# Kernel tuning notes

Hardware: AMD Instinct MI355X
Metric: run time of the kernel (lower is better)

The kernel has to match this reference:

```python
import jax, jax.numpy as jnp
import numpy as np
from jax.scipy.stats import norm

N_TOK, D_MODEL, N_EXP, N_SEL = 16384, 4096, 16, 4
NOISE_EPS = 0.01
LOSS_LAMBDA = 0.01


def setup_inputs() -> dict:
    key = jax.random.key(0)
    kx, k1, k2, kn, kz = jax.random.split(key, 5)
    x = jax.random.normal(kx, (N_TOK, D_MODEL), dtype=jnp.float32)
    w1 = jax.random.normal(k1, (N_EXP, D_MODEL), dtype=jnp.float32) * 0.02
    w2 = jax.random.normal(k2, (N_EXP, N_EXP), dtype=jnp.float32) * 0.02
    wn = jax.random.normal(kn, (N_EXP, D_MODEL), dtype=jnp.float32) * 0.02
    noise = jax.random.normal(kz, (N_TOK, N_EXP), dtype=jnp.float32)
    return {"x": x, "w1": w1, "w2": w2, "wn": wn, "noise": noise}


def _cv_squared(v, eps=1e-10):
    # torch .var() is unbiased (ddof=1)
    return jnp.var(v, ddof=1) / (jnp.mean(v) ** 2 + eps)


def reference(x, w1, w2, wn, noise):
    # MLP gate: Linear(D->E, no bias) -> tanh -> Linear(E->E, no bias)
    logits_gate = jnp.einsum("te,fe->tf", jnp.tanh(jnp.einsum("td,ed->te", x, w1)), w2)
    noise_control = jax.nn.softplus(jnp.einsum("td,ed->te", x, wn)) + NOISE_EPS
    logits_noise = noise * noise_control
    logits = logits_gate + logits_noise  # [T, E]

    m = min(N_SEL + 1, N_EXP)  # k+1 values for threshold computation
    top_logits, top_indices = jax.lax.top_k(logits, m)  # [T, m]
    top_k_logits = top_logits[:, :N_SEL]
    top_k_indices = top_indices[:, :N_SEL]
    top_k_scores = jax.nn.softmax(top_k_logits, axis=1)  # [T, k]

    # importance: scatter top-k scores back to dense [T, E]
    rows = jnp.arange(N_TOK)[:, None]
    scores_filtered = jnp.zeros_like(logits).at[rows, top_k_indices].set(top_k_scores)
    importance = scores_filtered.sum(0)  # [E]

    # load: smooth estimator via Normal CDF (faithful to source, which
    # compares logits_noise against the in/out thresholds)
    threshold_if_in = top_logits[:, N_SEL:N_SEL + 1]       # (k+1)-th top value, [T,1]
    threshold_if_out = top_logits[:, N_SEL - 1:N_SEL]      # k-th top value, [T,1]
    is_in = logits_noise > threshold_if_in
    prob_if_in = norm.cdf((logits_gate - threshold_if_in) / noise_control)
    prob_if_out = norm.cdf((logits_gate - threshold_if_out) / noise_control)
    prob = jnp.where(is_in, prob_if_in, prob_if_out)
    load = prob.sum(0)  # [E]

    gate_loss = LOSS_LAMBDA * (_cv_squared(importance) + _cv_squared(load))
    return top_k_indices, top_k_scores, gate_loss
```

## Files before the change

kernel.cpp:

```cpp
#include <hip/hip_runtime.h>
#include <math.h>

#define N_TOK   16384
#define D_MODEL 4096
#define N_EXP   16
#define N_SEL   4
#define WELEM   (N_EXP * D_MODEL)

typedef __bf16 bf16x8 __attribute__((ext_vector_type(8)));
typedef float  f32x4  __attribute__((ext_vector_type(4)));

#define MFMA(a, b, c) __builtin_amdgcn_mfma_f32_16x16x32_bf16((a), (b), (c), 0, 0, 0)

__global__ __launch_bounds__(256) void wprep_kernel(const float* __restrict__ w1,
                                                    const float* __restrict__ wn,
                                                    __bf16* __restrict__ wbuf,
                                                    float* __restrict__ g_acc)
{
    const int i = blockIdx.x * 256 + threadIdx.x;
    if (blockIdx.x == 0 && threadIdx.x < 2 * N_EXP) g_acc[threadIdx.x] = 0.f;
    {
        const float v = w1[i];
        const __bf16 h = (__bf16)v;  const float r1 = v - (float)h;
        const __bf16 m = (__bf16)r1; const float r2 = r1 - (float)m;
        wbuf[i] = h; wbuf[WELEM + i] = m; wbuf[2 * WELEM + i] = (__bf16)r2;
    }
    {
        const float v = wn[i];
        const __bf16 h = (__bf16)v;  const float r1 = v - (float)h;
        const __bf16 m = (__bf16)r1; const float r2 = r1 - (float)m;
        wbuf[3 * WELEM + i] = h; wbuf[4 * WELEM + i] = m; wbuf[5 * WELEM + i] = (__bf16)r2;
    }
}

__global__ __launch_bounds__(512, 8) void gate_kernel(
    const float* __restrict__ x, const __bf16* __restrict__ wbuf,
    const float* __restrict__ w2, const float* __restrict__ noise,
    float* __restrict__ out, float* __restrict__ g_imp, float* __restrict__ g_load)
{
    __shared__ float red[8][16][32];
    __shared__ float dsum[16][32];
    __shared__ float s_imp[N_EXP], s_ld[N_EXP];

    const int tid  = threadIdx.x;
    const int lane = tid & 63;
    const int wv   = tid >> 6;
    const int ml   = lane & 15;
    const int q    = lane >> 4;
    const int t0   = blockIdx.x * 16;

    const __bf16* w1h = wbuf;
    const __bf16* w1m = wbuf + WELEM;
    const __bf16* w1l = wbuf + 2 * WELEM;
    const __bf16* wnh = wbuf + 3 * WELEM;
    const __bf16* wnm = wbuf + 4 * WELEM;
    const __bf16* wnl = wbuf + 5 * WELEM;

    const size_t xoff = (size_t)(t0 + ml) * D_MODEL + wv * 512 + q * 8;
    const int    woff = ml * D_MODEL + wv * 512 + q * 8;

    f32x4 c1 = {0.f, 0.f, 0.f, 0.f};
    f32x4 c2 = {0.f, 0.f, 0.f, 0.f};

    #pragma unroll 2
    for (int it = 0; it < 16; ++it) {
        const int ko = it * 32;
        const float4 xa = *(const float4*)(x + xoff + ko);
        const float4 xb = *(const float4*)(x + xoff + ko + 4);
        const bf16x8 a1h = *(const bf16x8*)(w1h + woff + ko);
        const bf16x8 a1m = *(const bf16x8*)(w1m + woff + ko);
        const bf16x8 a1l = *(const bf16x8*)(w1l + woff + ko);
        const bf16x8 a2h = *(const bf16x8*)(wnh + woff + ko);
        const bf16x8 a2m = *(const bf16x8*)(wnm + woff + ko);
        const bf16x8 a2l = *(const bf16x8*)(wnl + woff + ko);

        const float xv[8] = {xa.x, xa.y, xa.z, xa.w, xb.x, xb.y, xb.z, xb.w};
        bf16x8 xh, xm8, xl;
        #pragma unroll
        for (int j = 0; j < 8; ++j) {
            const float v  = xv[j];
            const __bf16 h = (__bf16)v;   const float r1 = v - (float)h;
            const __bf16 md = (__bf16)r1; const float r2 = r1 - (float)md;
            xh[j] = h; xm8[j] = md; xl[j] = (__bf16)r2;
        }

        c1 = MFMA(a1h, xh, c1);  c1 = MFMA(a1h, xm8, c1); c1 = MFMA(a1m, xh, c1);
        c1 = MFMA(a1h, xl, c1);  c1 = MFMA(a1l, xh, c1);  c1 = MFMA(a1m, xm8, c1);
        c2 = MFMA(a2h, xh, c2);  c2 = MFMA(a2h, xm8, c2); c2 = MFMA(a2m, xh, c2);
        c2 = MFMA(a2h, xl, c2);  c2 = MFMA(a2l, xh, c2);  c2 = MFMA(a2m, xm8, c2);
    }

    #pragma unroll
    for (int r = 0; r < 4; ++r) {
        red[wv][ml][q * 4 + r]      = c1[r];
        red[wv][ml][16 + q * 4 + r] = c2[r];
    }
    __syncthreads();

    {
        const int tk = tid >> 5, o = tid & 31;
        float s = 0.f;
        #pragma unroll
        for (int w = 0; w < 8; ++w) s += red[w][tk][o];
        dsum[tk][o] = s;
    }
    if (tid < N_EXP) { s_imp[tid] = 0.f; s_ld[tid] = 0.f; }
    __syncthreads();

    if (tid < 16) {
        const int t = t0 + tid;
        float dot[32];
        #pragma unroll
        for (int e = 0; e < 32; ++e) dot[e] = dsum[tid][e];

        float th[N_EXP], nc[N_EXP];
        #pragma unroll
        for (int e = 0; e < N_EXP; ++e) th[e] = tanhf(dot[e]);
        #pragma unroll
        for (int e = 0; e < N_EXP; ++e) {
            const float v = dot[N_EXP + e];
            nc[e] = fmaxf(v, 0.f) + log1pf(expf(-fabsf(v))) + 0.01f;
        }

        float lg[N_EXP];
        #pragma unroll
        for (int f = 0; f < N_EXP; ++f) {
            float s = 0.f;
            #pragma unroll
            for (int e = 0; e < N_EXP; ++e) s = fmaf(th[e], w2[f * 16 + e], s);
            lg[f] = s;
        }

        float ln[N_EXP], v[N_EXP];
        {
            const float4* nz = (const float4*)(noise + (size_t)t * 16);
            const float4 n0 = nz[0], n1 = nz[1], n2 = nz[2], n3 = nz[3];
            const float nzv[16] = {n0.x, n0.y, n0.z, n0.w, n1.x, n1.y, n1.z, n1.w,
                                   n2.x, n2.y, n2.z, n2.w, n3.x, n3.y, n3.z, n3.w};
            #pragma unroll
            for (int e = 0; e < N_EXP; ++e) {
                ln[e] = nzv[e] * nc[e];
                v[e]  = lg[e] + ln[e];
            }
        }

        float tv[5]; int ti[5];
        #pragma unroll
        for (int j = 0; j < 5; ++j) {
            float best = -INFINITY; int bi = 0;
            #pragma unroll
            for (int e = 0; e < N_EXP; ++e) {
                bool taken = false;
                #pragma unroll
                for (int jj = 0; jj < 5; ++jj)
                    if (jj < j) taken = taken || (ti[jj] == e);
                if (!taken && v[e] > best) { best = v[e]; bi = e; }
            }
            tv[j] = best; ti[j] = bi;
        }

        const float mx = tv[0];
        float ex[4], ssum = 0.f;
        #pragma unroll
        for (int j = 0; j < 4; ++j) { ex[j] = expf(tv[j] - mx); ssum += ex[j]; }
        const float inv = 1.f / ssum;
        float sc[4];
        #pragma unroll
        for (int j = 0; j < 4; ++j) sc[j] = ex[j] * inv;

        #pragma unroll
        for (int j = 0; j < 4; ++j) atomicAdd(&s_imp[ti[j]], sc[j]);

        const float thr_in = tv[4], thr_out = tv[3];
        #pragma unroll
        for (int e = 0; e < N_EXP; ++e) {
            const bool  is_in = ln[e] > thr_in;
            const float thr   = is_in ? thr_in : thr_out;
            const float z     = (lg[e] - thr) / nc[e];
            const float prob  = 0.5f * (1.f + erff(z * 0.70710678118654752f));
            atomicAdd(&s_ld[e], prob);
        }

        ((float4*)out)[t] = make_float4((float)ti[0], (float)ti[1],
                                        (float)ti[2], (float)ti[3]);
        ((float4*)(out + N_TOK * N_SEL))[t] = make_float4(sc[0], sc[1], sc[2], sc[3]);
    }
    __syncthreads();
    if (tid < N_EXP)            atomicAdd(&g_imp[tid], s_imp[tid]);
    else if (tid < 2 * N_EXP)   atomicAdd(&g_load[tid - N_EXP], s_ld[tid - N_EXP]);
}

__global__ void loss_kernel(const float* __restrict__ g_imp,
                            const float* __restrict__ g_load,
                            float* __restrict__ out)
{
    if (threadIdx.x == 0 && blockIdx.x == 0) {
        double mi = 0.0, ml = 0.0;
        for (int e = 0; e < N_EXP; ++e) { mi += g_imp[e]; ml += g_load[e]; }
        mi /= N_EXP; ml /= N_EXP;
        double vi = 0.0, vl = 0.0;
        for (int e = 0; e < N_EXP; ++e) {
            const double di = g_imp[e] - mi;  vi += di * di;
            const double dl = g_load[e] - ml; vl += dl * dl;
        }
        vi /= (N_EXP - 1); vl /= (N_EXP - 1);
        const double ci = vi / (mi * mi + 1e-10);
        const double cl = vl / (ml * ml + 1e-10);
        out[N_TOK * N_SEL * 2] = (float)(0.01 * (ci + cl));
    }
}

extern "C" void kernel_launch(void* const* d_in, const int* in_sizes, int n_in,
                              void* d_out, int out_size, void* d_ws, size_t ws_size,
                              hipStream_t stream)
{
    const float* x     = (const float*)d_in[0];
    const float* w1    = (const float*)d_in[1];
    const float* w2    = (const float*)d_in[2];
    const float* wn    = (const float*)d_in[3];
    const float* noise = (const float*)d_in[4];
    float* out = (float*)d_out;

    __bf16* wbuf  = (__bf16*)d_ws;
    float*  g_imp = (float*)((char*)d_ws + (1 << 20));
    float*  g_load = g_imp + N_EXP;

    wprep_kernel<<<WELEM / 256, 256, 0, stream>>>(w1, wn, wbuf, g_imp);
    gate_kernel<<<N_TOK / 16, 512, 0, stream>>>(x, wbuf, w2, noise, out,
                                                g_imp, g_load);
    loss_kernel<<<1, 64, 0, stream>>>(g_imp, g_load, out);
}
```

Baseline: 463.3 us.

## Process two 16-token tiles per block to reuse loaded weight fragments

```diff
diff --git a/kernel.cpp b/kernel.cpp
--- a/kernel.cpp
+++ b/kernel.cpp
@@ -6,6 +6,7 @@
 #define N_EXP   16
 #define N_SEL   4
 #define WELEM   (N_EXP * D_MODEL)
+#define TILES   2
 
 typedef __bf16 bf16x8 __attribute__((ext_vector_type(8)));
 typedef float  f32x4  __attribute__((ext_vector_type(4)));
@@ -33,13 +34,26 @@
     }
 }
 
-__global__ __launch_bounds__(512, 8) void gate_kernel(
+__device__ __forceinline__ void split8(const float4 a, const float4 b,
+                                       bf16x8& h, bf16x8& m, bf16x8& l)
+{
+    const float v[8] = {a.x, a.y, a.z, a.w, b.x, b.y, b.z, b.w};
+    #pragma unroll
+    for (int j = 0; j < 8; ++j) {
+        const float vv = v[j];
+        const __bf16 hh = (__bf16)vv;  const float r1 = vv - (float)hh;
+        const __bf16 mm = (__bf16)r1;  const float r2 = r1 - (float)mm;
+        h[j] = hh; m[j] = mm; l[j] = (__bf16)r2;
+    }
+}
+
+__global__ __launch_bounds__(512, 4) void gate_kernel(
     const float* __restrict__ x, const __bf16* __restrict__ wbuf,
     const float* __restrict__ w2, const float* __restrict__ noise,
     float* __restrict__ out, float* __restrict__ g_imp, float* __restrict__ g_load)
 {
-    __shared__ float red[8][16][32];
-    __shared__ float dsum[16][32];
+    __shared__ float red[8][TILES][16][33];
+    __shared__ float dsum[TILES][16][33];
     __shared__ float s_imp[N_EXP], s_ld[N_EXP];
 
     const int tid  = threadIdx.x;
@@ -47,7 +61,7 @@
     const int wv   = tid >> 6;
     const int ml   = lane & 15;
     const int q    = lane >> 4;
-    const int t0   = blockIdx.x * 16;
+    const int t0   = blockIdx.x * (TILES * 16);
 
     const __bf16* w1h = wbuf;
     const __bf16* w1m = wbuf + WELEM;
@@ -56,62 +70,75 @@
     const __bf16* wnm = wbuf + 4 * WELEM;
     const __bf16* wnl = wbuf + 5 * WELEM;
 
-    const size_t xoff = (size_t)(t0 + ml) * D_MODEL + wv * 512 + q * 8;
-    const int    woff = ml * D_MODEL + wv * 512 + q * 8;
-
-    f32x4 c1 = {0.f, 0.f, 0.f, 0.f};
-    f32x4 c2 = {0.f, 0.f, 0.f, 0.f};
+    const size_t xoff0 = (size_t)(t0 + ml) * D_MODEL + wv * 512 + q * 8;
+    const size_t xoff1 = xoff0 + (size_t)16 * D_MODEL;
+    const int    woff  = ml * D_MODEL + wv * 512 + q * 8;
+
+    f32x4 c1[TILES], c2[TILES];
+    #pragma unroll
+    for (int tt = 0; tt < TILES; ++tt) {
+        c1[tt] = (f32x4){0.f, 0.f, 0.f, 0.f};
+        c2[tt] = (f32x4){0.f, 0.f, 0.f, 0.f};
+    }
 
     #pragma unroll 2
     for (int it = 0; it < 16; ++it) {
         const int ko = it * 32;
-        const float4 xa = *(const float4*)(x + xoff + ko);
-        const float4 xb = *(const float4*)(x + xoff + ko + 4);
         const bf16x8 a1h = *(const bf16x8*)(w1h + woff + ko);
         const bf16x8 a1m = *(const bf16x8*)(w1m + woff + ko);
         const bf16x8 a1l = *(const bf16x8*)(w1l + woff + ko);
         const bf16x8 a2h = *(const bf16x8*)(wnh + woff + ko);
         const bf16x8 a2m = *(const bf16x8*)(wnm + woff + ko);
         const bf16x8 a2l = *(const bf16x8*)(wnl + woff + ko);
-
-        const float xv[8] = {xa.x, xa.y, xa.z, xa.w, xb.x, xb.y, xb.z, xb.w};
-        bf16x8 xh, xm8, xl;
-        #pragma unroll
-        for (int j = 0; j < 8; ++j) {
-            const float v  = xv[j];
-            const __bf16 h = (__bf16)v;   const float r1 = v - (float)h;
-            const __bf16 md = (__bf16)r1; const float r2 = r1 - (float)md;
-            xh[j] = h; xm8[j] = md; xl[j] = (__bf16)r2;
-        }
-
-        c1 = MFMA(a1h, xh, c1);  c1 = MFMA(a1h, xm8, c1); c1 = MFMA(a1m, xh, c1);
-        c1 = MFMA(a1h, xl, c1);  c1 = MFMA(a1l, xh, c1);  c1 = MFMA(a1m, xm8, c1);
-        c2 = MFMA(a2h, xh, c2);  c2 = MFMA(a2h, xm8, c2); c2 = MFMA(a2m, xh, c2);
-        c2 = MFMA(a2h, xl, c2);  c2 = MFMA(a2l, xh, c2);  c2 = MFMA(a2m, xm8, c2);
+        const float4 xa0 = *(const float4*)(x + xoff0 + ko);
+        const float4 xb0 = *(const float4*)(x + xoff0 + ko + 4);
+        const float4 xa1 = *(const float4*)(x + xoff1 + ko);
+        const float4 xb1 = *(const float4*)(x + xoff1 + ko + 4);
+
+        bf16x8 xh0, xm0, xl0, xh1, xm1, xl1;
+        split8(xa0, xb0, xh0, xm0, xl0);
+        split8(xa1, xb1, xh1, xm1, xl1);
+
+        c1[0] = MFMA(a1h, xh0, c1[0]);  c2[0] = MFMA(a2h, xh0, c2[0]);
+        c1[1] = MFMA(a1h, xh1, c1[1]);  c2[1] = MFMA(a2h, xh1, c2[1]);
+        c1[0] = MFMA(a1h, xm0, c1[0]);  c2[0] = MFMA(a2h, xm0, c2[0]);
+        c1[1] = MFMA(a1h, xm1, c1[1]);  c2[1] = MFMA(a2h, xm1, c2[1]);
+        c1[0] = MFMA(a1m, xh0, c1[0]);  c2[0] = MFMA(a2m, xh0, c2[0]);
+        c1[1] = MFMA(a1m, xh1, c1[1]);  c2[1] = MFMA(a2m, xh1, c2[1]);
+        c1[0] = MFMA(a1h, xl0, c1[0]);  c2[0] = MFMA(a2h, xl0, c2[0]);
+        c1[1] = MFMA(a1h, xl1, c1[1]);  c2[1] = MFMA(a2h, xl1, c2[1]);
+        c1[0] = MFMA(a1l, xh0, c1[0]);  c2[0] = MFMA(a2l, xh0, c2[0]);
+        c1[1] = MFMA(a1l, xh1, c1[1]);  c2[1] = MFMA(a2l, xh1, c2[1]);
+        c1[0] = MFMA(a1m, xm0, c1[0]);  c2[0] = MFMA(a2m, xm0, c2[0]);
+        c1[1] = MFMA(a1m, xm1, c1[1]);  c2[1] = MFMA(a2m, xm1, c2[1]);
     }
 
     #pragma unroll
-    for (int r = 0; r < 4; ++r) {
-        red[wv][ml][q * 4 + r]      = c1[r];
-        red[wv][ml][16 + q * 4 + r] = c2[r];
+    for (int tt = 0; tt < TILES; ++tt) {
+        #pragma unroll
+        for (int r = 0; r < 4; ++r) {
+            red[wv][tt][ml][q * 4 + r]      = c1[tt][r];
+            red[wv][tt][ml][16 + q * 4 + r] = c2[tt][r];
+        }
     }
     __syncthreads();
 
-    {
-        const int tk = tid >> 5, o = tid & 31;
+    for (int idx = tid; idx < TILES * 512; idx += 512) {
+        const int tt = idx >> 9, tk = (idx >> 5) & 15, o = idx & 31;
         float s = 0.f;
         #pragma unroll
-        for (int w = 0; w < 8; ++w) s += red[w][tk][o];
-        dsum[tk][o] = s;
+        for (int w = 0; w < 8; ++w) s += red[w][tt][tk][o];
+        dsum[tt][tk][o] = s;
     }
     if (tid < N_EXP) { s_imp[tid] = 0.f; s_ld[tid] = 0.f; }
     __syncthreads();
 
-    if (tid < 16) {
+    if (tid < TILES * 16) {
+        const int tt = tid >> 4, tk = tid & 15;
         const int t = t0 + tid;
         float dot[32];
         #pragma unroll
-        for (int e = 0; e < 32; ++e) dot[e] = dsum[tid][e];
+        for (int e = 0; e < 32; ++e) dot[e] = dsum[tt][tk][e];
 
         float th[N_EXP], nc[N_EXP];
         #pragma unroll
@@ -226,7 +253,7 @@
     float*  g_load = g_imp + N_EXP;
 
     wprep_kernel<<<WELEM / 256, 256, 0, stream>>>(w1, wn, wbuf, g_imp);
-    gate_kernel<<<N_TOK / 16, 512, 0, stream>>>(x, wbuf, w2, noise, out,
-                                                g_imp, g_load);
+    gate_kernel<<<N_TOK / (TILES * 16), 512, 0, stream>>>(x, wbuf, w2, noise, out,
+                                                          g_imp, g_load);
     loss_kernel<<<1, 64, 0, stream>>>(g_imp, g_load, out);
 }
```

After: 406.6 us. 1.14x faster.
